# Optimization experiments

Measured on AMD Instinct MI355X. Metric: run time of the kernel, lower is better.

## Reference

```python
import jax, jax.numpy as jnp
import numpy as np

HEADS, DH, HID, EDGE_D = 8, 16, 128, 32  # heads, head_dim, hidden_dim, edge_dim
N, E = 50000, 800000


def _ln(x, w, b):
    mu = jnp.mean(x, axis=-1, keepdims=True)
    var = jnp.var(x, axis=-1, keepdims=True)
    return (x - mu) * jax.lax.rsqrt(var + 1e-5) * w + b


def setup_inputs() -> dict:
    key = jax.random.key(0)
    ks = jax.random.split(key, 16)
    lin = lambda k, fi, fo: (jax.random.normal(k, (fi, fo), jnp.float32) / np.sqrt(fi).astype(np.float32))
    inp = {
        'x': jax.random.normal(ks[0], (N, HID), jnp.float32),
        'edge_index': jax.random.randint(ks[1], (2, E), 0, N, jnp.int32),
        'edge_attr': jax.random.normal(ks[2], (E, EDGE_D), jnp.float32),
        'Wq': lin(ks[3], HID, HID), 'bq': jnp.zeros((HID,), jnp.float32),
        'Wk': lin(ks[4], HID, HID), 'bk': jnp.zeros((HID,), jnp.float32),
        'Wv': lin(ks[5], HID, HID), 'bv': jnp.zeros((HID,), jnp.float32),
        'We': lin(ks[6], EDGE_D, HID), 'be': jnp.zeros((HID,), jnp.float32),
        'Wskip': lin(ks[7], HID, HID), 'bskip': jnp.zeros((HID,), jnp.float32),
        'ln1_w': jnp.ones((HID,), jnp.float32), 'ln1_b': jnp.zeros((HID,), jnp.float32),
        'W1': lin(ks[8], HID, 4 * HID), 'b1': jnp.zeros((4 * HID,), jnp.float32),
        'W2': lin(ks[9], 4 * HID, HID), 'b2': jnp.zeros((HID,), jnp.float32),
        'ln2_w': jnp.ones((HID,), jnp.float32), 'ln2_b': jnp.zeros((HID,), jnp.float32),
    }
    return inp


def reference(x, edge_index, edge_attr, Wq, bq, Wk, bk, Wv, bv, We, be,
              Wskip, bskip, ln1_w, ln1_b, W1, b1, W2, b2, ln2_w, ln2_b):
    n = x.shape[0]
    src, dst = edge_index[0], edge_index[1]

    h = _ln(x, ln1_w, ln1_b)
    # projections, then per-edge gathers -> [E, H, Dh]
    q = (h @ Wq + bq)[dst].reshape(-1, HEADS, DH)
    k = (h @ Wk + bk)[src].reshape(-1, HEADS, DH)
    v = (h @ Wv + bv)[src].reshape(-1, HEADS, DH)
    e = (edge_attr @ We + be).reshape(-1, HEADS, DH)
    k = k + e
    v = v + e

    alpha = jnp.einsum('ehd,ehd->eh', q, k) / np.sqrt(DH).astype(np.float32)  # [E, H]
    # segment softmax over destination nodes (PyG softmax semantics)
    amax = jax.ops.segment_max(alpha, dst, num_segments=n)
    amax = jnp.where(jnp.isfinite(amax), amax, 0.0)
    expa = jnp.exp(alpha - amax[dst])
    denom = jax.ops.segment_sum(expa, dst, num_segments=n)
    alpha = expa / (denom[dst] + 1e-16)

    msg = jax.ops.segment_sum(alpha[..., None] * v, dst, num_segments=n)  # [N, H, Dh]
    conv_out = msg.reshape(n, HID) + h @ Wskip + bskip  # root_weight skip

    x = x + conv_out
    h2 = _ln(x, ln2_w, ln2_b)
    ffn = jax.nn.gelu(h2 @ W1 + b1, approximate=False) @ W2 + b2
    return x + ffn
```

## Files before the change

### kernel.cpp

```cpp
#include <hip/hip_runtime.h>
#include <math.h>

#define HID 128
#define EDGE_D 32
#define SC 0.36067376f

typedef unsigned short u16;
typedef unsigned int u32;
typedef __bf16 bf16x8 __attribute__((ext_vector_type(8)));
typedef float f32x4 __attribute__((ext_vector_type(4)));
typedef u32 u32x4 __attribute__((ext_vector_type(4)));
typedef u32 u32x2 __attribute__((ext_vector_type(2)));

static __device__ __forceinline__ u16 f2bf(float f) {
  u32 u = __float_as_uint(f);
  u += 0x7fffu + ((u >> 16) & 1u);
  return (u16)(u >> 16);
}
static __device__ __forceinline__ u32 pack2(float a, float b) {
  return (u32)f2bf(a) | ((u32)f2bf(b) << 16);
}
static __device__ __forceinline__ float bflo(u32 w) { return __uint_as_float(w << 16); }
static __device__ __forceinline__ float bfhi(u32 w) { return __uint_as_float(w & 0xffff0000u); }
static __device__ __forceinline__ float grp16_sum(float x) {
  x += __int_as_float(__builtin_amdgcn_mov_dpp(__float_as_int(x), 0x128, 0xf, 0xf, true));
  x += __int_as_float(__builtin_amdgcn_mov_dpp(__float_as_int(x), 0x124, 0xf, 0xf, true));
  x += __int_as_float(__builtin_amdgcn_mov_dpp(__float_as_int(x), 0x122, 0xf, 0xf, true));
  x += __int_as_float(__builtin_amdgcn_mov_dpp(__float_as_int(x), 0x121, 0xf, 0xf, true));
  return x;
}
static __device__ __forceinline__ float wave_allreduce_sum(float v) {
#pragma unroll
  for (int off = 32; off > 0; off >>= 1) v += __shfl_xor(v, off);
  return v;
}

__global__ __launch_bounds__(256) void ln_kernel(const float* __restrict__ in,
                                                 u16* __restrict__ out,
                                                 const float* __restrict__ w,
                                                 const float* __restrict__ b, int n) {
  int row0 = blockIdx.x * 4 + (threadIdx.x >> 6);
  int lane = threadIdx.x & 63;
  int stride = gridDim.x * 4;
  for (int row = row0; row < n; row += stride) {
    const float* p = in + (size_t)row * HID;
    float a = p[lane], c = p[lane + 64];
    float s = wave_allreduce_sum(a + c);
    float s2 = wave_allreduce_sum(a * a + c * c);
    float mean = s * (1.f / 128.f);
    float var = s2 * (1.f / 128.f) - mean * mean;
    float rs = rsqrtf(var + 1e-5f);
    u16* o = out + (size_t)row * HID;
    o[lane] = f2bf((a - mean) * rs * w[lane] + b[lane]);
    o[lane + 64] = f2bf((c - mean) * rs * w[lane + 64] + b[lane + 64]);
  }
}

__global__ __launch_bounds__(256) void convert_weights(
    const float* __restrict__ Wq, const float* __restrict__ Wk,
    const float* __restrict__ Wv, const float* __restrict__ Ws,
    const float* __restrict__ W1, const float* __restrict__ W2,
    const float* __restrict__ We, const float* __restrict__ bq,
    u16* __restrict__ WqkvsT, u16* __restrict__ W1T, u16* __restrict__ W2T,
    u16* __restrict__ WbdT, u16* __restrict__ WfoldT, float* __restrict__ bfold,
    int* __restrict__ cnt, int Nn) {
  int idx = blockIdx.x * 256 + threadIdx.x;
  if (idx < 65536) {
    int m = idx >> 7, k = idx & 127;
    const float* Wm = m < 128 ? Wq : m < 256 ? Wk : m < 384 ? Wv : Ws;
    WqkvsT[idx] = f2bf(Wm[k * 128 + (m & 127)]);
  } else if (idx < 131072) {
    int j = idx - 65536;
    int m = j >> 7, k = j & 127;
    W1T[j] = f2bf(W1[k * 512 + m]);
  } else if (idx < 196608) {
    int j = idx - 131072;
    int m = j >> 9, k = j & 511;
    W2T[j] = f2bf(W2[k * 128 + m]);
  } else if (idx < 229376) {
    int j = idx - 196608;
    int m = j >> 8, c = j & 255;
    WbdT[j] = ((c >> 5) == (m >> 4)) ? f2bf(We[(c & 31) * 128 + m]) : (u16)0;
  } else if (idx < 262144) {
    int j = idx - 229376;
    int m = j >> 7, k = j & 127;
    int base = (m >> 5) * 16;
    const float* wq = Wq + k * 128 + base;
    const float* we = We + (m & 31) * 128 + base;
    float s = 0.f;
#pragma unroll
    for (int t = 0; t < 16; t++) s = fmaf(wq[t], we[t], s);
    WfoldT[j] = f2bf(s * SC);
  } else if (idx < 262400) {
    int m = idx - 262144;
    int base = (m >> 5) * 16;
    const float* we = We + (m & 31) * 128 + base;
    float s = 0.f;
#pragma unroll
    for (int t = 0; t < 16; t++) s = fmaf(bq[base + t], we[t], s);
    bfold[m] = s * SC;
  } else if (idx < 262400 + Nn) {
    cnt[idx - 262400] = 0;
  }
}

#define GSTAGE(buf, kc)                                                        \
  {                                                                            \
    _Pragma("unroll") for (int i = 0; i < 2; i++) {                            \
      int idx = i * 256 + t;                                                   \
      int row = idx >> 2, c4 = idx & 3;                                        \
      __builtin_amdgcn_global_load_lds(                                        \
          (const __attribute__((address_space(1))) u32*)(A + (size_t)(r0 + row) * K + (kc) + c4 * 8), \
          (__attribute__((address_space(3))) u32*)&As[buf][idx * 8], 16, 0, 0);\
      __builtin_amdgcn_global_load_lds(                                        \
          (const __attribute__((address_space(1))) u32*)(Bt + (size_t)(c0 + row) * K + (kc) + c4 * 8), \
          (__attribute__((address_space(3))) u32*)&Bs[buf][idx * 8], 16, 0, 0);\
    }                                                                          \
  }

#define GEMM_CORE                                                              \
  constexpr int NT = K / 32;                                                   \
  GSTAGE(0, 0)                                                                 \
  __syncthreads();                                                             \
  _Pragma("unroll") for (int tt = 0; tt < NT; tt++) {                          \
    if (tt + 1 < NT) GSTAGE((tt + 1) & 1, (tt + 1) * 32)                       \
    bf16x8 a0 = *(const bf16x8*)&As[tt & 1][(w * 32 + sr) * 32 + g * 8];       \
    bf16x8 a1 = *(const bf16x8*)&As[tt & 1][(w * 32 + 16 + sr) * 32 + g * 8];  \
    _Pragma("unroll") for (int nn = 0; nn < 8; nn++) {                         \
      bf16x8 b = *(const bf16x8*)&Bs[tt & 1][(nn * 16 + sr) * 32 + g * 8];     \
      acc[0][nn] = __builtin_amdgcn_mfma_f32_16x16x32_bf16(a0, b, acc[0][nn], 0, 0, 0); \
      acc[1][nn] = __builtin_amdgcn_mfma_f32_16x16x32_bf16(a1, b, acc[1][nn], 0, 0, 0); \
    }                                                                          \
    __syncthreads();                                                           \
  }

template <int EPI, int K>
__global__ __launch_bounds__(256) void gemm_bf16(
    const u16* __restrict__ A, const u16* __restrict__ BtQ,
    const u16* __restrict__ BtF, int n,
    const float* __restrict__ bias0, const float* __restrict__ bias1,
    const float* __restrict__ bias2, const float* __restrict__ bfold,
    float* __restrict__ of0, u32* __restrict__ opq, u32* __restrict__ pkv,
    u16* __restrict__ qweb16, u16* __restrict__ ob1,
    const float* __restrict__ addsrc) {
  __shared__ u16 As[2][128 * 32];
  __shared__ u16 Bs[2][128 * 32];
  int t = threadIdx.x;
  int w = t >> 6, lane = t & 63;
  int g = lane >> 4, sr = lane & 15;
  int r0 = blockIdx.x * 128;
  int c0;
  const u16* Bt;
  if (EPI == 0 && blockIdx.y >= 3) {
    c0 = (blockIdx.y - 3) * 128;
    Bt = BtF;
  } else {
    c0 = blockIdx.y * 128;
    Bt = BtQ;
  }
  f32x4 acc[2][8];
#pragma unroll
  for (int m = 0; m < 2; m++)
#pragma unroll
    for (int nn = 0; nn < 8; nn++) acc[m][nn] = {0.f, 0.f, 0.f, 0.f};

  GEMM_CORE

  if (EPI == 0 && blockIdx.y == 0) {
#pragma unroll
    for (int m = 0; m < 2; m++)
#pragma unroll
      for (int nn = 0; nn < 4; nn++)
#pragma unroll
        for (int j = 0; j < 4; j++) {
          int row = r0 + w * 32 + m * 16 + g * 4 + j;
          if (row < n) {
            int cj = nn * 16 + sr;
            opq[((size_t)row << 6) + cj] =
                pack2(acc[m][nn][j] + bias0[cj], acc[m][nn + 4][j] + bias0[cj + 64]);
          }
        }
    return;
  }
  if (EPI == 0 && blockIdx.y < 3) {
    const float* bp = blockIdx.y == 1 ? bias1 : bias2;
    int which = blockIdx.y - 1;
#pragma unroll
    for (int m = 0; m < 2; m++)
#pragma unroll
      for (int nn = 0; nn < 4; nn++)
#pragma unroll
        for (int j = 0; j < 4; j++) {
          int row = r0 + w * 32 + m * 16 + g * 4 + j;
          if (row < n) {
            int cj = nn * 16 + sr;
            pkv[((size_t)row << 7) + (cj << 1) + which] =
                pack2(acc[m][nn][j] + bp[cj], acc[m][nn + 4][j] + bp[cj + 64]);
          }
        }
    return;
  }
  if (EPI == 0) {
    const float* bf = bfold + c0;
#pragma unroll
    for (int m = 0; m < 2; m++)
#pragma unroll
      for (int nn = 0; nn < 4; nn++)
#pragma unroll
        for (int j = 0; j < 4; j++) {
          int row = r0 + w * 32 + m * 16 + g * 4 + j;
          if (row < n) {
            int cj = nn * 16 + sr;
            u16* qrow = qweb16 + ((size_t)row << 8) + c0;
            qrow[cj] = f2bf(acc[m][nn][j] + bf[cj]);
            qrow[cj + 64] = f2bf(acc[m][nn + 4][j] + bf[cj + 64]);
          }
        }
    return;
  }
#pragma unroll
  for (int m = 0; m < 2; m++)
#pragma unroll
    for (int nn = 0; nn < 8; nn++)
#pragma unroll
      for (int j = 0; j < 4; j++) {
        int row = r0 + w * 32 + m * 16 + g * 4 + j;
        if (row < n) {
          int cj = nn * 16 + sr;
          float val = acc[m][nn][j];
          if (EPI == 1) {
            int cjg = blockIdx.y * 128 + cj;
            float v2 = val + bias0[cjg];
            v2 = 0.5f * v2 * (1.f + erff(v2 * 0.70710678118f));
            ob1[(size_t)row * 512 + cjg] = f2bf(v2);
          } else {
            of0[(size_t)row * HID + cj] = val + bias0[cj] + addsrc[(size_t)row * HID + cj];
          }
        }
      }
}

__global__ __launch_bounds__(256) void gemm_bd_fin(
    const u16* __restrict__ Aw, const u16* __restrict__ BtW,
    const u16* __restrict__ Ah, const u16* __restrict__ BtS, int n,
    const float* __restrict__ x, const u32* __restrict__ msgb,
    const float* __restrict__ be, const float* __restrict__ bskip,
    const float* __restrict__ lnw, const float* __restrict__ lnb,
    float* __restrict__ x1, u16* __restrict__ h2) {
  __shared__ u16 As[2][128 * 32];
  __shared__ u16 Bs[2][128 * 32];
  int t = threadIdx.x;
  int w = t >> 6, lane = t & 63;
  int g = lane >> 4, sr = lane & 15;
  int r0 = blockIdx.x * 128;
  int c0 = 0;
  f32x4 acc[2][8];
#pragma unroll
  for (int m = 0; m < 2; m++)
#pragma unroll
    for (int nn = 0; nn < 8; nn++) acc[m][nn] = {0.f, 0.f, 0.f, 0.f};

  {
    const u16* A = Aw;
    const u16* Bt = BtW;
    constexpr int K = 256;
    GEMM_CORE
  }
  {
    const u16* A = Ah;
    const u16* Bt = BtS;
    constexpr int K = 128;
    GEMM_CORE
  }

  float becol[8], wcol[8], bcol[8], bscol[8];
#pragma unroll
  for (int nn = 0; nn < 8; nn++) {
    int c = nn * 16 + sr;
    becol[nn] = be[c];
    bscol[nn] = bskip[c];
    wcol[nn] = lnw[c];
    bcol[nn] = lnb[c];
  }
#pragma unroll
  for (int m = 0; m < 2; m++)
#pragma unroll
    for (int j = 0; j < 4; j++) {
      int row = r0 + w * 32 + m * 16 + g * 4 + j;
      if (row < n) {
        const float* xr = x + (size_t)row * HID;
        const u32* mr = msgb + ((size_t)row << 6);
        float* x1r = x1 + (size_t)row * HID;
        u32 mw[4];
#pragma unroll
        for (int nn = 0; nn < 4; nn++) mw[nn] = mr[nn * 16 + sr];
        float tv[8];
        float s = 0.f, s2 = 0.f;
#pragma unroll
        for (int nn = 0; nn < 8; nn++) {
          int c = nn * 16 + sr;
          float mval = nn < 4 ? bflo(mw[nn]) : bfhi(mw[nn - 4]);
          float t1 = xr[c] + mval + acc[m][nn][j] + becol[nn] + bscol[nn];
          tv[nn] = t1;
          s += t1;
          s2 = fmaf(t1, t1, s2);
        }
        s = grp16_sum(s);
        s2 = grp16_sum(s2);
        float mean = s * (1.f / 128.f);
        float var = s2 * (1.f / 128.f) - mean * mean;
        float rs = rsqrtf(var + 1e-5f);
        u16* h2r = h2 + (size_t)row * HID;
#pragma unroll
        for (int nn = 0; nn < 8; nn++) {
          int c = nn * 16 + sr;
          x1r[c] = tv[nn];
          h2r[c] = f2bf((tv[nn] - mean) * rs * wcol[nn] + bcol[nn]);
        }
      }
    }
}

__global__ __launch_bounds__(256) void hist_kernel(const int* __restrict__ dstp,
                                                   int* __restrict__ cnt, int E) {
  int i = blockIdx.x * blockDim.x + threadIdx.x;
  int stride = gridDim.x * blockDim.x;
  for (; i < E; i += stride) atomicAdd(&cnt[dstp[i]], 1);
}

__global__ __launch_bounds__(256) void scan_partial(const int* __restrict__ cnt,
                                                    int* __restrict__ bs, int N) {
  __shared__ int sd[256];
  int idx = blockIdx.x * 256 + threadIdx.x;
  sd[threadIdx.x] = (idx < N) ? cnt[idx] : 0;
  __syncthreads();
  for (int s = 128; s > 0; s >>= 1) {
    if (threadIdx.x < s) sd[threadIdx.x] += sd[threadIdx.x + s];
    __syncthreads();
  }
  if (threadIdx.x == 0) bs[blockIdx.x] = sd[0];
}

__global__ __launch_bounds__(256) void scan_final(const int* __restrict__ cnt,
                                                  const int* __restrict__ bs,
                                                  int* __restrict__ offs,
                                                  int* __restrict__ woff, int N,
                                                  int nb) {
  __shared__ int sb[256];
  __shared__ int sd[256];
  int t = threadIdx.x;
  sb[t] = (t < nb && t < (int)blockIdx.x) ? bs[t] : 0;
  __syncthreads();
  for (int s = 128; s > 0; s >>= 1) {
    if (t < s) sb[t] += sb[t + s];
    __syncthreads();
  }
  int base = sb[0];
  int idx = blockIdx.x * 256 + t;
  int v = (idx < N) ? cnt[idx] : 0;
  sd[t] = v;
  __syncthreads();
  for (int s = 1; s < 256; s <<= 1) {
    int add = (t >= s) ? sd[t - s] : 0;
    __syncthreads();
    sd[t] += add;
    __syncthreads();
  }
  if (idx < N) {
    int ex = sd[t] - v + base;
    offs[idx] = ex;
    woff[idx] = ex;
  }
}

__global__ __launch_bounds__(256) void scatter_kernel(const int* __restrict__ ei,
                                                      int* __restrict__ woff,
                                                      int2* __restrict__ sorted,
                                                      int E) {
  int i = blockIdx.x * blockDim.x + threadIdx.x;
  int stride = gridDim.x * blockDim.x;
  for (; i < E; i += stride) {
    int src = ei[i];
    int dst = ei[E + i];
    int pos = atomicAdd(&woff[dst], 1);
    sorted[pos] = make_int2(src, i);
  }
}

#define ISSUE4(P, base_)                                                       \
  {                                                                            \
    _Pragma("unroll") for (int jj = 0; jj < 4; jj++) {                         \
      int sj = min(base_ + jj, segn - 1);                                      \
      int sxx = __builtin_amdgcn_readlane(seRx, sj);                           \
      int syy = __builtin_amdgcn_readlane(seRy, sj);                           \
      P##kv[jj] = *(const u32x2*)(pkv + ((size_t)sxx << 7) + (lane << 1));     \
      P##ea[jj] = *(const float2*)(eaf + ((size_t)syy << 5) + 2 * sr);         \
    }                                                                          \
  }

#define COMP4(P, base_)                                                        \
  {                                                                            \
    _Pragma("unroll") for (int jj = 0; jj < 4; jj++) {                         \
      u32 kx = P##kv[jj].x, ky = P##kv[jj].y;                                  \
      float ex = P##ea[jj].x, ey = P##ea[jj].y;                                \
      float k0 = bflo(kx), k1 = bfhi(kx);                                      \
      float v0f = bflo(ky), v1f = bfhi(ky);                                    \
      float p0 = fmaf(q0C, k0, fmaf(qw0x, ex, qw0y * ey));                     \
      float p1 = fmaf(q1C, k1, fmaf(qw1x, ex, qw1y * ey));                     \
      p0 = grp16_sum(p0) + qb0C;                                               \
      p1 = grp16_sum(p1) + qb1C;                                               \
      bool val_ = (base_ + jj) < segn;                                         \
      float w1 = val_ ? __builtin_amdgcn_exp2f(p0) : 0.f;                      \
      float w2 = val_ ? __builtin_amdgcn_exp2f(p1) : 0.f;                      \
      l1 += w1;                                                                \
      l2 += w2;                                                                \
      a0 = fmaf(w1, v0f, a0);                                                  \
      a1 = fmaf(w2, v1f, a1);                                                  \
      wa00 = fmaf(w1, ex, wa00);                                               \
      wa01 = fmaf(w1, ey, wa01);                                               \
      wa10 = fmaf(w2, ex, wa10);                                               \
      wa11 = fmaf(w2, ey, wa11);                                               \
    }                                                                          \
  }

__global__ __launch_bounds__(256) void fused_edge(
    const int* __restrict__ offs, const int* __restrict__ cnt,
    const int2* __restrict__ sorted, const float* __restrict__ eaf,
    const float* __restrict__ be, const u32* __restrict__ pq,
    const u32* __restrict__ pkv, const u16* __restrict__ qweb16,
    u32* __restrict__ msgb, u32* __restrict__ weab, int Nn, int Etot) {
  int lane = threadIdx.x & 63;
  int w = threadIdx.x >> 6;
  int g = lane >> 4, sr = lane & 15;
  int wid = blockIdx.x * 4 + w;
  int nw = gridDim.x * 4;
  int per = (Nn + nw - 1) / nw;
  int n0 = wid * per;
  int n1 = min(Nn, n0 + per);
  if (n0 >= n1) return;
  int nn = n1 - n0;

  float be0 = be[lane], be1 = be[lane + 64];

  int ml = min(lane, nn - 1);
  int myBeg = offs[n0 + ml];
  int myCnt = cnt[n0 + ml];

  int beg = __builtin_amdgcn_readlane(myBeg, 0);
  int num = __builtin_amdgcn_readlane(myCnt, 0);
  int2 se2 = sorted[min(beg + min(lane, max(num - 1, 0)), Etot - 1)];
  int seCx = se2.x, seCy = se2.y;
  u32 pqC = pq[(size_t)n0 * 64 + lane];
  u32 qwb0C = *(const u32*)(qweb16 + ((size_t)n0 << 8) + g * 32 + 2 * sr);
  u32 qwb1C = *(const u32*)(qweb16 + ((size_t)n0 << 8) + (4 + g) * 32 + 2 * sr);

  for (int ni = 0; ni < nn; ni++) {
    int node = n0 + ni;
    int begX = 0, numX = 0, seXx = 0, seXy = 0;
    u32 pqX = 0, qwb0X = 0, qwb1X = 0;
    if (ni + 1 < nn) {
      begX = __builtin_amdgcn_readlane(myBeg, ni + 1);
      numX = __builtin_amdgcn_readlane(myCnt, ni + 1);
      int2 sx = sorted[min(begX + min(lane, max(numX - 1, 0)), Etot - 1)];
      seXx = sx.x;
      seXy = sx.y;
      pqX = pq[(size_t)(node + 1) * 64 + lane];
      qwb0X = *(const u32*)(qweb16 + ((size_t)(node + 1) << 8) + g * 32 + 2 * sr);
      qwb1X = *(const u32*)(qweb16 + ((size_t)(node + 1) << 8) + (4 + g) * 32 + 2 * sr);
    }
    float q0C = bflo(pqC) * SC, q1C = bfhi(pqC) * SC;
    float qw0x = bflo(qwb0C), qw0y = bfhi(qwb0C);
    float qw1x = bflo(qwb1C), qw1y = bfhi(qwb1C);
    float qb0C = grp16_sum(q0C * be0);
    float qb1C = grp16_sum(q1C * be1);
    float l1 = 0.f, l2 = 0.f, a0 = 0.f, a1 = 0.f;
    float wa00 = 0.f, wa01 = 0.f, wa10 = 0.f, wa11 = 0.f;
    if (num > 0) {
      int cb = 0;
      int seRx = seCx, seRy = seCy;
      while (true) {
        int segn = min(num - cb, 64);
        u32x2 Akv[4], Bkv[4];
        float2 Aea[4], Bea[4];
        ISSUE4(A, 0)
        for (int c = 0; c < segn; c += 8) {
          ISSUE4(B, c + 4)
          COMP4(A, c)
          ISSUE4(A, c + 8)
          COMP4(B, c + 4)
        }
        cb += 64;
        if (cb >= num) break;
        int rem = num - cb;
        int2 sn = sorted[min(beg + cb + min(lane, rem - 1), Etot - 1)];
        seRx = sn.x;
        seRy = sn.y;
      }
    }
    float inv1 = 1.f / (l1 + 1e-30f), inv2 = 1.f / (l2 + 1e-30f);
    if (num > 0) {
      msgb[((size_t)node << 6) + lane] = pack2(a0 * inv1, a1 * inv2);
    } else {
      msgb[((size_t)node << 6) + lane] = pack2(-be0, -be1);
    }
    weab[(size_t)node * 128 + g * 16 + sr] = pack2(wa00 * inv1, wa01 * inv1);
    weab[(size_t)node * 128 + 64 + g * 16 + sr] = pack2(wa10 * inv2, wa11 * inv2);
    beg = begX;
    num = numX;
    seCx = seXx;
    seCy = seXy;
    pqC = pqX;
    qwb0C = qwb0X;
    qwb1C = qwb1X;
  }
}

extern "C" void kernel_launch(void* const* d_in, const int* in_sizes, int n_in,
                              void* d_out, int out_size, void* d_ws, size_t ws_size,
                              hipStream_t stream) {
  const float* x = (const float*)d_in[0];
  const int* ei = (const int*)d_in[1];
  const float* ea = (const float*)d_in[2];
  const float* Wq = (const float*)d_in[3];
  const float* bq = (const float*)d_in[4];
  const float* Wk = (const float*)d_in[5];
  const float* bk = (const float*)d_in[6];
  const float* Wv = (const float*)d_in[7];
  const float* bv = (const float*)d_in[8];
  const float* We = (const float*)d_in[9];
  const float* be = (const float*)d_in[10];
  const float* Wskip = (const float*)d_in[11];
  const float* bskip = (const float*)d_in[12];
  const float* ln1w = (const float*)d_in[13];
  const float* ln1b = (const float*)d_in[14];
  const float* W1 = (const float*)d_in[15];
  const float* b1p = (const float*)d_in[16];
  const float* W2 = (const float*)d_in[17];
  const float* b2p = (const float*)d_in[18];
  const float* ln2w = (const float*)d_in[19];
  const float* ln2b = (const float*)d_in[20];

  int N = in_sizes[0] / HID;
  int E = in_sizes[1] / 2;
  size_t nf = (size_t)N * HID;

  float* ws = (float*)d_ws;
  size_t off = 0;
  u16* h_bf = (u16*)(ws + off); off += nf / 2;
  u32* pq = (u32*)(ws + off); off += nf / 2;
  u32* pkv = (u32*)(ws + off); off += nf;
  float* skipx1 = ws + off; off += nf;
  u32* msgb = (u32*)(ws + off); off += nf / 2;
  u32* weab = (u32*)(ws + off); off += nf;
  u16* qweb16 = (u16*)(ws + off); off += nf;
  int2* sorted = (int2*)(ws + off); off += (size_t)E * 2;
  int* cnt = (int*)(ws + off); off += N;
  int* offs = (int*)(ws + off); off += N;
  int* woff = (int*)(ws + off); off += N;
  int* bs = (int*)(ws + off); off += 256;
  u16* WqkvsT = (u16*)(ws + off); off += 32768;
  u16* W1T = (u16*)(ws + off); off += 32768;
  u16* W2T = (u16*)(ws + off); off += 32768;
  u16* WbdT = (u16*)(ws + off); off += 16384;
  u16* WfoldT = (u16*)(ws + off); off += 16384;
  float* bfold = ws + off; off += 256;
  u16* h2o = (u16*)pq;
  u16* tbf = (u16*)msgb;

  convert_weights<<<1221, 256, 0, stream>>>(Wq, Wk, Wv, Wskip, W1, W2, We, bq,
                                            WqkvsT, W1T, W2T, WbdT, WfoldT,
                                            bfold, cnt, N);

  int ln_blocks = (N + 3) / 4;
  ln_kernel<<<ln_blocks, 256, 0, stream>>>(x, h_bf, ln1w, ln1b, N);

  dim3 gq((N + 127) / 128, 5);
  gemm_bf16<0, 128><<<gq, 256, 0, stream>>>(h_bf, WqkvsT, WfoldT, N, bq, bk, bv,
                                            bfold, nullptr, pq, pkv, qweb16,
                                            nullptr, nullptr);

  int nb = (N + 255) / 256;
  hist_kernel<<<1024, 256, 0, stream>>>(ei + E, cnt, E);
  scan_partial<<<nb, 256, 0, stream>>>(cnt, bs, N);
  scan_final<<<nb, 256, 0, stream>>>(cnt, bs, offs, woff, N, nb);
  scatter_kernel<<<1024, 256, 0, stream>>>(ei, woff, sorted, E);

  int fe_blocks = (N + 15) / 16;
  fused_edge<<<fe_blocks, 256, 0, stream>>>(offs, cnt, sorted, ea, be, pq, pkv,
                                            qweb16, msgb, weab, N, E);

  dim3 ge((N + 127) / 128, 1);
  gemm_bd_fin<<<ge, 256, 0, stream>>>((const u16*)weab, WbdT, h_bf,
                                      WqkvsT + 384 * 128, N, x, msgb, be, bskip,
                                      ln2w, ln2b, skipx1, h2o);

  dim3 gf1((N + 127) / 128, 4);
  gemm_bf16<1, 128><<<gf1, 256, 0, stream>>>(h2o, W1T, nullptr, N, b1p, nullptr,
                                             nullptr, nullptr, nullptr, nullptr,
                                             nullptr, nullptr, tbf, nullptr);
  dim3 gf2((N + 127) / 128, 1);
  gemm_bf16<2, 512><<<gf2, 256, 0, stream>>>(tbf, W2T, nullptr, N, b2p, nullptr,
                                             nullptr, nullptr, (float*)d_out,
                                             nullptr, nullptr, nullptr, nullptr,
                                             skipx1);
}
```

Before: 408.2 us.

## Fuse FFN up and down projections into one kernel, store residual in bf16

Replaces the two FFN GEMM launches with a single kernel that computes the GELU hidden chunk per 64-row tile in LDS and immediately multiplies it by W2. This avoids writing and reading the 512-wide intermediate through global memory. The residual x1 is also stored as bf16 instead of fp32 to cut traffic, at some cost in output precision. Weights are read straight from global/L2 without shared-memory staging, which may limit MFMA efficiency.

New measurement: 491.0 us. 20.3% more time.

```diff
diff --git a/kernel.cpp b/kernel.cpp
--- a/kernel.cpp
+++ b/kernel.cpp
@@ -22,6 +22,9 @@
 }
 static __device__ __forceinline__ float bflo(u32 w) { return __uint_as_float(w << 16); }
 static __device__ __forceinline__ float bfhi(u32 w) { return __uint_as_float(w & 0xffff0000u); }
+static __device__ __forceinline__ float bf2f16(u16 b) {
+  return __uint_as_float(((u32)b) << 16);
+}
 static __device__ __forceinline__ float grp16_sum(float x) {
   x += __int_as_float(__builtin_amdgcn_mov_dpp(__float_as_int(x), 0x128, 0xf, 0xf, true));
   x += __int_as_float(__builtin_amdgcn_mov_dpp(__float_as_int(x), 0x124, 0xf, 0xf, true));
@@ -140,9 +143,7 @@
     const u16* __restrict__ BtF, int n,
     const float* __restrict__ bias0, const float* __restrict__ bias1,
     const float* __restrict__ bias2, const float* __restrict__ bfold,
-    float* __restrict__ of0, u32* __restrict__ opq, u32* __restrict__ pkv,
-    u16* __restrict__ qweb16, u16* __restrict__ ob1,
-    const float* __restrict__ addsrc) {
+    u32* __restrict__ opq, u32* __restrict__ pkv, u16* __restrict__ qweb16) {
   __shared__ u16 As[2][128 * 32];
   __shared__ u16 Bs[2][128 * 32];
   int t = threadIdx.x;
@@ -151,7 +152,7 @@
   int r0 = blockIdx.x * 128;
   int c0;
   const u16* Bt;
-  if (EPI == 0 && blockIdx.y >= 3) {
+  if (blockIdx.y >= 3) {
     c0 = (blockIdx.y - 3) * 128;
     Bt = BtF;
   } else {
@@ -166,7 +167,7 @@
 
   GEMM_CORE
 
-  if (EPI == 0 && blockIdx.y == 0) {
+  if (blockIdx.y == 0) {
 #pragma unroll
     for (int m = 0; m < 2; m++)
 #pragma unroll
@@ -182,7 +183,7 @@
         }
     return;
   }
-  if (EPI == 0 && blockIdx.y < 3) {
+  if (blockIdx.y < 3) {
     const float* bp = blockIdx.y == 1 ? bias1 : bias2;
     int which = blockIdx.y - 1;
 #pragma unroll
@@ -200,42 +201,19 @@
         }
     return;
   }
-  if (EPI == 0) {
-    const float* bf = bfold + c0;
-#pragma unroll
-    for (int m = 0; m < 2; m++)
-#pragma unroll
-      for (int nn = 0; nn < 4; nn++)
-#pragma unroll
-        for (int j = 0; j < 4; j++) {
-          int row = r0 + w * 32 + m * 16 + g * 4 + j;
-          if (row < n) {
-            int cj = nn * 16 + sr;
-            u16* qrow = qweb16 + ((size_t)row << 8) + c0;
-            qrow[cj] = f2bf(acc[m][nn][j] + bf[cj]);
-            qrow[cj + 64] = f2bf(acc[m][nn + 4][j] + bf[cj + 64]);
-          }
-        }
-    return;
-  }
+  const float* bf = bfold + c0;
 #pragma unroll
   for (int m = 0; m < 2; m++)
 #pragma unroll
-    for (int nn = 0; nn < 8; nn++)
+    for (int nn = 0; nn < 4; nn++)
 #pragma unroll
       for (int j = 0; j < 4; j++) {
         int row = r0 + w * 32 + m * 16 + g * 4 + j;
         if (row < n) {
           int cj = nn * 16 + sr;
-          float val = acc[m][nn][j];
-          if (EPI == 1) {
-            int cjg = blockIdx.y * 128 + cj;
-            float v2 = val + bias0[cjg];
-            v2 = 0.5f * v2 * (1.f + erff(v2 * 0.70710678118f));
-            ob1[(size_t)row * 512 + cjg] = f2bf(v2);
-          } else {
-            of0[(size_t)row * HID + cj] = val + bias0[cj] + addsrc[(size_t)row * HID + cj];
-          }
+          u16* qrow = qweb16 + ((size_t)row << 8) + c0;
+          qrow[cj] = f2bf(acc[m][nn][j] + bf[cj]);
+          qrow[cj + 64] = f2bf(acc[m][nn + 4][j] + bf[cj + 64]);
         }
       }
 }
@@ -246,7 +224,7 @@
     const float* __restrict__ x, const u32* __restrict__ msgb,
     const float* __restrict__ be, const float* __restrict__ bskip,
     const float* __restrict__ lnw, const float* __restrict__ lnb,
-    float* __restrict__ x1, u16* __restrict__ h2) {
+    u16* __restrict__ x1b, u16* __restrict__ h2) {
   __shared__ u16 As[2][128 * 32];
   __shared__ u16 Bs[2][128 * 32];
   int t = threadIdx.x;
@@ -290,7 +268,7 @@
       if (row < n) {
         const float* xr = x + (size_t)row * HID;
         const u32* mr = msgb + ((size_t)row << 6);
-        float* x1r = x1 + (size_t)row * HID;
+        u16* x1r = x1b + (size_t)row * HID;
         u32 mw[4];
 #pragma unroll
         for (int nn = 0; nn < 4; nn++) mw[nn] = mr[nn * 16 + sr];
@@ -314,11 +292,75 @@
 #pragma unroll
         for (int nn = 0; nn < 8; nn++) {
           int c = nn * 16 + sr;
-          x1r[c] = tv[nn];
+          x1r[c] = f2bf(tv[nn]);
           h2r[c] = f2bf((tv[nn] - mean) * rs * wcol[nn] + bcol[nn]);
         }
       }
     }
+}
+
+__global__ __launch_bounds__(256) void fused_ffn(
+    const u16* __restrict__ h2, const u16* __restrict__ W1T,
+    const u16* __restrict__ W2T, const float* __restrict__ b1,
+    const float* __restrict__ b2, const u16* __restrict__ x1b,
+    float* __restrict__ out, int n) {
+  __shared__ u16 tch[64 * 136];
+  int t = threadIdx.x;
+  int w = t >> 6, lane = t & 63;
+  int g = lane >> 4, sr = lane & 15;
+  int r0 = blockIdx.x * 64;
+  int rowA = min(r0 + w * 16 + sr, n - 1);
+  f32x4 accO[8];
+#pragma unroll
+  for (int nn = 0; nn < 8; nn++) accO[nn] = {0.f, 0.f, 0.f, 0.f};
+#pragma unroll
+  for (int c = 0; c < 4; c++) {
+    f32x4 acc1[8];
+#pragma unroll
+    for (int nn = 0; nn < 8; nn++) acc1[nn] = {0.f, 0.f, 0.f, 0.f};
+#pragma unroll
+    for (int tt = 0; tt < 4; tt++) {
+      bf16x8 a0 = *(const bf16x8*)(h2 + (size_t)rowA * 128 + tt * 32 + g * 8);
+#pragma unroll
+      for (int nn = 0; nn < 8; nn++) {
+        bf16x8 b = *(const bf16x8*)(W1T + (size_t)(c * 128 + nn * 16 + sr) * 128 +
+                                    tt * 32 + g * 8);
+        acc1[nn] = __builtin_amdgcn_mfma_f32_16x16x32_bf16(a0, b, acc1[nn], 0, 0, 0);
+      }
+    }
+#pragma unroll
+    for (int nn = 0; nn < 8; nn++) {
+      float bc = b1[c * 128 + nn * 16 + sr];
+#pragma unroll
+      for (int j = 0; j < 4; j++) {
+        float v = acc1[nn][j] + bc;
+        v = 0.5f * v * (1.f + erff(v * 0.70710678118f));
+        tch[(w * 16 + g * 4 + j) * 136 + nn * 16 + sr] = f2bf(v);
+      }
+    }
+#pragma unroll
+    for (int tt = 0; tt < 4; tt++) {
+      bf16x8 a0 = *(const bf16x8*)&tch[(w * 16 + sr) * 136 + tt * 32 + g * 8];
+#pragma unroll
+      for (int nn = 0; nn < 8; nn++) {
+        bf16x8 b = *(const bf16x8*)(W2T + (size_t)(nn * 16 + sr) * 512 + c * 128 +
+                                    tt * 32 + g * 8);
+        accO[nn] = __builtin_amdgcn_mfma_f32_16x16x32_bf16(a0, b, accO[nn], 0, 0, 0);
+      }
+    }
+  }
+#pragma unroll
+  for (int nn = 0; nn < 8; nn++) {
+#pragma unroll
+    for (int j = 0; j < 4; j++) {
+      int r = r0 + w * 16 + g * 4 + j;
+      if (r < n) {
+        int cj = nn * 16 + sr;
+        out[(size_t)r * 128 + cj] =
+            accO[nn][j] + b2[cj] + bf2f16(x1b[(size_t)r * 128 + cj]);
+      }
+    }
+  }
 }
 
 __global__ __launch_bounds__(256) void hist_kernel(const int* __restrict__ dstp,
@@ -549,7 +591,7 @@
   u16* h_bf = (u16*)(ws + off); off += nf / 2;
   u32* pq = (u32*)(ws + off); off += nf / 2;
   u32* pkv = (u32*)(ws + off); off += nf;
-  float* skipx1 = ws + off; off += nf;
+  u16* x1b = (u16*)(ws + off); off += nf / 2;
   u32* msgb = (u32*)(ws + off); off += nf / 2;
   u32* weab = (u32*)(ws + off); off += nf;
   u16* qweb16 = (u16*)(ws + off); off += nf;
@@ -565,7 +607,6 @@
   u16* WfoldT = (u16*)(ws + off); off += 16384;
   float* bfold = ws + off; off += 256;
   u16* h2o = (u16*)pq;
-  u16* tbf = (u16*)msgb;
 
   convert_weights<<<1221, 256, 0, stream>>>(Wq, Wk, Wv, Wskip, W1, W2, We, bq,
                                             WqkvsT, W1T, W2T, WbdT, WfoldT,
@@ -576,8 +617,7 @@
 
   dim3 gq((N + 127) / 128, 5);
   gemm_bf16<0, 128><<<gq, 256, 0, stream>>>(h_bf, WqkvsT, WfoldT, N, bq, bk, bv,
-                                            bfold, nullptr, pq, pkv, qweb16,
-                                            nullptr, nullptr);
+                                            bfold, pq, pkv, qweb16);
 
   int nb = (N + 255) / 256;
   hist_kernel<<<1024, 256, 0, stream>>>(ei + E, cnt, E);
@@ -592,15 +632,8 @@
   dim3 ge((N + 127) / 128, 1);
   gemm_bd_fin<<<ge, 256, 0, stream>>>((const u16*)weab, WbdT, h_bf,
                                       WqkvsT + 384 * 128, N, x, msgb, be, bskip,
-                                      ln2w, ln2b, skipx1, h2o);
-
-  dim3 gf1((N + 127) / 128, 4);
-  gemm_bf16<1, 128><<<gf1, 256, 0, stream>>>(h2o, W1T, nullptr, N, b1p, nullptr,
-                                             nullptr, nullptr, nullptr, nullptr,
-                                             nullptr, nullptr, tbf, nullptr);
-  dim3 gf2((N + 127) / 128, 1);
-  gemm_bf16<2, 512><<<gf2, 256, 0, stream>>>(tbf, W2T, nullptr, N, b2p, nullptr,
-                                             nullptr, nullptr, (float*)d_out,
-                                             nullptr, nullptr, nullptr, nullptr,
-                                             skipx1);
-}
+                                      ln2w, ln2b, x1b, h2o);
+
+  fused_ffn<<<(N + 63) / 64, 256, 0, stream>>>(h2o, W1T, W2T, b1p, b2p, x1b,
+                                               (float*)d_out, N);
+}
```
